# Optimization experiments

Hardware: AMD Instinct MI355X
Metric: run time of the kernel (lower is better)

The kernel has to match this reference:

```python
import jax, jax.numpy as jnp
import numpy as np


def _block(x, src, dst, edge_attr, Wl, bl, Wu, bu):
    # PyG MessagePassing (flow source_to_target): x_i = x[dst], x_j = x[src]
    z = jnp.concatenate([x[dst], x[src], edge_attr], axis=-1)
    m = jax.nn.leaky_relu(z @ Wl + bl)  # default negative_slope = 0.01
    agg = jax.ops.segment_sum(m, dst, num_segments=x.shape[0])  # aggr='add'
    return agg + x @ Wu + bu  # residual upsample


def _rodrigues(axis, ang):
    # axis [...,3] (unit), ang [...] -> rotation matrices [...,3,3]
    ax, ay, az = axis[..., 0], axis[..., 1], axis[..., 2]
    zero = jnp.zeros_like(ax)
    K = jnp.stack([
        jnp.stack([zero, -az, ay], axis=-1),
        jnp.stack([az, zero, -ax], axis=-1),
        jnp.stack([-ay, ax, zero], axis=-1),
    ], axis=-2)
    s = jnp.sin(ang)[..., None, None]
    c = jnp.cos(ang)[..., None, None]
    I = jnp.eye(3, dtype=axis.dtype)
    return I + s * K + (1.0 - c) * (K @ K)


def _fk(ang, parent, offset, G, axis):
    # axis-angle forward kinematics over G graphs of J joints each
    J = ang.shape[0] // G
    a = ang.reshape(G, J)
    ax = axis.reshape(G, J, 3)
    off = offset.reshape(G, J, 3)
    par = parent.reshape(G, J)
    Rl = _rodrigues(ax, a)  # [G,J,3,3] local rotations
    gid = jnp.arange(G)
    pos = jnp.zeros((G, J, 3), ang.dtype)
    rot = jnp.zeros((G, J, 3, 3), ang.dtype)
    for j in range(J):  # J=18 fixed, parents topologically ordered
        p = par[:, j]
        root = (p < 0)[:, None]
        ps = jnp.clip(p, 0, J - 1)
        pr = rot[gid, ps]  # [G,3,3]
        pp = pos[gid, ps]  # [G,3]
        rj = jnp.where(root[..., None], Rl[:, j], pr @ Rl[:, j])
        pj = jnp.where(root, off[:, j], pp + jnp.einsum('gij,gj->gi', pr, off[:, j]))
        rot = rot.at[:, j].set(rj)
        pos = pos.at[:, j].set(pj)
    return pos.reshape(G * J, 3)


def setup_inputs():
    key = jax.random.key(0)
    ks = jax.random.split(key, 48)
    B, Js, Es, Jt, Et = 8192, 17, 16, 18, 17
    f32 = jnp.float32

    def rn(k, shape, scale=1.0):
        return jax.random.normal(k, shape, dtype=f32) * scale

    def lin(k, fin, fout):
        k1, k2 = jax.random.split(k)
        s = 1.0 / float(np.sqrt(fin))
        return rn(k1, (fin, fout), s), rn(k2, (fout,), s)

    offs = np.arange(B)[:, None]
    js = np.arange(Es)
    ei_s = jnp.asarray(np.stack([(offs * Js + js).ravel(), (offs * Js + js + 1).ravel()]), dtype=jnp.int32)
    jt = np.arange(Et)
    ei_t = jnp.asarray(np.stack([(offs * Jt + jt).ravel(), (offs * Jt + jt + 1).ravel()]), dtype=jnp.int32)
    parent = jnp.asarray(np.tile(np.arange(-1, Jt - 1), B), dtype=jnp.int32)
    u = jax.random.uniform(ks[0], (B * Jt, 1), dtype=f32) * 1.5 + 0.1
    axis = rn(ks[1], (B * Jt, 3))
    axis = axis / (jnp.linalg.norm(axis, axis=-1, keepdims=True) + 1e-8)

    inp = {
        'l_hand_x': rn(ks[2], (B * Js, 3)),
        'r_hand_x': rn(ks[3], (B * Js, 3)),
        'l_hand_edge_index': ei_s,
        'r_hand_edge_index': ei_s,
        'l_hand_edge_attr': rn(ks[4], (B * Es, 3)),
        'r_hand_edge_attr': rn(ks[5], (B * Es, 3)),
        'hand_edge_index': ei_t,
        'hand_edge_attr': rn(ks[6], (B * Et, 6)),
        'hand_lower': -u,
        'hand_upper': u,
        'hand_offset': rn(ks[7], (B * Jt, 3), 0.05),
        'hand_parent': parent,
        'hand_axis': axis,
        'num_graphs': B,
    }
    blocks = [('enc1', 3, 16, 3), ('enc2', 16, 32, 3), ('enc3', 32, 64, 3),
              ('dec1', 66, 32, 6), ('dec2', 32, 16, 6), ('dec3', 16, 1, 6)]
    i = 8
    for nm, cin, cout, ed in blocks:
        w, b = lin(ks[i], 2 * cin + ed, cout); i += 1
        inp[nm + '_lw'], inp[nm + '_lb'] = w, b
        w, b = lin(ks[i], cin, cout); i += 1
        inp[nm + '_uw'], inp[nm + '_ub'] = w, b
    w, b = lin(ks[i], Js * 64, Jt * 64)
    inp['trans_w'], inp['trans_b'] = w, b
    return inp


def reference(l_hand_x, r_hand_x, l_hand_edge_index, r_hand_edge_index, l_hand_edge_attr, r_hand_edge_attr, hand_edge_index, hand_edge_attr, hand_lower, hand_upper, hand_offset, hand_parent, hand_axis, num_graphs, enc1_lw, enc1_lb, enc1_uw, enc1_ub, enc2_lw, enc2_lb, enc2_uw, enc2_ub, enc3_lw, enc3_lb, enc3_uw, enc3_ub, trans_w, trans_b, dec1_lw, dec1_lb, dec1_uw, dec1_ub, dec2_lw, dec2_lb, dec2_uw, dec2_ub, dec3_lw, dec3_lb, dec3_uw, dec3_ub):
    # ---- encode ----
    x = jnp.concatenate([l_hand_x, r_hand_x], axis=0)
    ei = jnp.concatenate([l_hand_edge_index, r_hand_edge_index + l_hand_x.shape[0]], axis=1)
    ea = jnp.concatenate([l_hand_edge_attr, r_hand_edge_attr], axis=0)
    s, d = ei[0], ei[1]
    h = _block(x, s, d, ea, enc1_lw, enc1_lb, enc1_uw, enc1_ub)
    h = _block(h, s, d, ea, enc2_lw, enc2_lb, enc2_uw, enc2_ub)
    h = _block(h, s, d, ea, enc3_lw, enc3_lb, enc3_uw, enc3_ub)
    G2 = 2 * num_graphs
    z = jnp.tanh(h.reshape(G2, -1) @ trans_w + trans_b).reshape(-1, 64)
    # ---- decode ----
    half = z.shape[0] // 2
    ei2 = jnp.concatenate([hand_edge_index, hand_edge_index + half], axis=1)
    ea2 = jnp.concatenate([hand_edge_attr, hand_edge_attr], axis=0)
    lo = jnp.concatenate([hand_lower, hand_lower], axis=0)
    up = jnp.concatenate([hand_upper, hand_upper], axis=0)
    off = jnp.concatenate([hand_offset, hand_offset], axis=0)
    par = jnp.concatenate([hand_parent, hand_parent], axis=0)
    ax = jnp.concatenate([hand_axis, hand_axis], axis=0)
    s2, d2 = ei2[0], ei2[1]
    xd = jnp.concatenate([z, lo, up], axis=1)  # [2B*18, 66]
    hd = _block(xd, s2, d2, ea2, dec1_lw, dec1_lb, dec1_uw, dec1_ub)
    hd = _block(hd, s2, d2, ea2, dec2_lw, dec2_lb, dec2_uw, dec2_ub)
    hd = jnp.tanh(_block(hd, s2, d2, ea2, dec3_lw, dec3_lb, dec3_uw, dec3_ub))
    ang = lo + (up - lo) * (hd + 1.0) / 2.0
    pos = _fk(ang, par, off, G2, ax)
    hn = ang.shape[0] // 2
    return (z, ang[:hn], pos[:hn], ang[hn:], pos[hn:])
```

## Files before the change

### kernel.cpp

```cpp
#include <hip/hip_runtime.h>
#include <hip/hip_bf16.h>
#include <stdint.h>


#define ZSIZE 18874368
#define AHALF 147456
#define PHALF 442368

#define WS_AE 0
#define WS_WT 35651584
#define WS_PACK 38158336

#define P_E1 0
#define P_E2 1280
#define P_E3 5888
#define P_D1 19200
#define P_D2 29952

using f32x4 = __attribute__((ext_vector_type(4))) float;
using f16x8 = __attribute__((ext_vector_type(8))) _Float16;
using f16x4 = __attribute__((ext_vector_type(4))) _Float16;

__device__ __forceinline__ float tanh_fast(float x) {
    x = fminf(40.f, fmaxf(-40.f, x));
    float e = __expf(2.f * x);
    return (e - 1.f) * __builtin_amdgcn_rcpf(e + 1.f);
}
__device__ __forceinline__ float lrelu(float x) { return x > 0.f ? x : 0.01f * x; }

__device__ __forceinline__ void gload_lds16(const void* g, void* l) {
    __builtin_amdgcn_global_load_lds(
        (__attribute__((address_space(1))) unsigned int*)g,
        (__attribute__((address_space(3))) unsigned int*)l, 16, 0, 0);
}

__global__ __launch_bounds__(256) void prep_all(
    _Float16* __restrict__ P,
    const float* __restrict__ W, _Float16* __restrict__ Wt,
    const float* __restrict__ e1l, const float* __restrict__ e1u,
    const float* __restrict__ e2l, const float* __restrict__ e2u,
    const float* __restrict__ e3l, const float* __restrict__ e3u,
    const float* __restrict__ d1l, const float* __restrict__ d1u,
    const float* __restrict__ d2l, const float* __restrict__ d2u)
{
    __shared__ float t[32][33];
    const int b = blockIdx.x;
    const int tid = threadIdx.x;

    if (b < 260) {
        const int p = b / 52;
        const int e = (b - p * 52) * 256 + tid;
        int Np, Kp, KpP, N, din, ed, K0, off; const float *Wl, *Wu;
        switch (p) {
          case 0:  Np=32;  Kp=32;  KpP=40;  N=16; din=3;  ed=3; K0=8;  off=P_E1; Wl=e1l; Wu=e1u; break;
          case 1:  Np=64;  Kp=64;  KpP=72;  N=32; din=16; ed=3; K0=24; off=P_E2; Wl=e2l; Wu=e2u; break;
          case 2:  Np=128; Kp=96;  KpP=104; N=64; din=32; ed=3; K0=40; off=P_E3; Wl=e3l; Wu=e3u; break;
          case 3:  Np=64;  Kp=160; KpP=168; N=32; din=66; ed=6; K0=72; off=P_D1; Wl=d1l; Wu=d1u; break;
          default: Np=32;  Kp=96;  KpP=104; N=16; din=32; ed=6; K0=40; off=P_D2; Wl=d2l; Wu=d2u; break;
        }
        if (e >= Np * KpP) return;
        const int n = e / KpP, k = e - n * KpP;
        float v = 0.f;
        if (k < Kp) {
            if (n < N) {
                if (k < din)                          v = Wl[k * N + n];
                else if (k >= K0 && k < K0 + din)     v = Wl[(din + k - K0) * N + n];
                else if (k >= 2*K0 && k < 2*K0 + ed)  v = Wl[(2*din + k - 2*K0) * N + n];
            } else {
                if (k < din) v = Wu[k * N + (n - N)];
            }
        }
        P[off + e] = (_Float16)v;
    } else {
        const int pb = b - 260;
        const int bx = pb % 34, by = pb / 34;
        const int k0 = bx * 32, n0 = by * 32;
        const int tx = tid & 31, ty = tid >> 5;
        for (int i = ty; i < 32; i += 8)
            t[i][tx] = W[(size_t)(k0 + i) * 1152 + n0 + tx];
        __syncthreads();
        for (int i = ty; i < 32; i += 8)
            Wt[(size_t)(n0 + i) * 1088 + k0 + tx] = (_Float16)t[tx][i];
    }
}

#define E_SX 0
#define E_EA 1280
#define E_H1 3840
#define E_H2 7680
#define E_WQ 14080

__global__ __launch_bounds__(256) void enc_kernel(
    const float* __restrict__ lx,  const float* __restrict__ rx,
    const float* __restrict__ lea, const float* __restrict__ rea,
    const float* __restrict__ b1l, const float* __restrict__ b1u,
    const float* __restrict__ b2l, const float* __restrict__ b2u,
    const float* __restrict__ b3l, const float* __restrict__ b3u,
    const _Float16* __restrict__ pack,
    _Float16* __restrict__ Ae)
{
    __shared__ __align__(16) _Float16 sm[27392];
    __shared__ float sb[224];

    const int tid = threadIdx.x;
    const int wave = tid >> 6, lane = tid & 63;
    const int quad = lane >> 4, l16 = lane & 15;
    const int g2b = blockIdx.x * 8;

    for (int i = tid; i < 7040; i += 256) ((uint32_t*)sm)[i] = 0u;
    { uint4* d = (uint4*)&sm[E_WQ]; const uint4* s = (const uint4*)(pack + P_E1);
      for (int i = tid; i < 736; i += 256) d[i] = s[i]; }
    for (int i = tid; i < 16; i += 256) { sb[i] = b1l[i]; sb[16 + i] = b1u[i]; }
    for (int i = tid; i < 32; i += 256) { sb[32 + i] = b2l[i]; sb[64 + i] = b2u[i]; }
    for (int i = tid; i < 64; i += 256) { sb[96 + i] = b3l[i]; sb[160 + i] = b3u[i]; }
    __syncthreads();

    const float* xs = (g2b < 8192) ? lx  + (size_t)g2b * 51 : rx  + (size_t)(g2b - 8192) * 51;
    const float* es = (g2b < 8192) ? lea + (size_t)g2b * 48 : rea + (size_t)(g2b - 8192) * 48;
    for (int i = tid; i < 408; i += 256) {
        int g = i / 51, j = i - g * 51, node = j / 3, c = j - node * 3;
        sm[E_SX + (g * 20 + node) * 8 + c] = (_Float16)xs[i];
    }
    for (int i = tid; i < 384; i += 256) {
        int g = i / 48, j = i - g * 48, node = j / 3, c = j - node * 3;
        sm[E_EA + (g * 20 + node) * 16 + c] = (_Float16)es[i];
    }
    __syncthreads();

    int mts[3] = { wave, wave + 4, wave + 8 };
    const bool has[3] = { true, true, wave < 2 };
    int gN[3], ndN[3], npN[3];
    #pragma unroll
    for (int t = 0; t < 3; t++) {
        const int r16 = mts[t] * 16 + l16;
        gN[t] = r16 / 20; ndN[t] = r16 - gN[t] * 20;
        npN[t] = ndN[t] ? ndN[t] - 1 : 0;
    }

    {
        f32x4 acc[3][2];
        #pragma unroll
        for (int t = 0; t < 3; t++)
            #pragma unroll
            for (int n = 0; n < 2; n++)
                #pragma unroll
                for (int r = 0; r < 4; r++) acc[t][n][r] = 0.f;
        f16x8 bfr[2];
        #pragma unroll
        for (int nt = 0; nt < 2; nt++)
            bfr[nt] = *(const f16x8*)&sm[E_WQ + (nt * 16 + l16) * 40 + quad * 8];
        #pragma unroll
        for (int t = 0; t < 3; t++) if (has[t]) {
            const int aD = E_SX + (gN[t] * 20 + ndN[t]) * 8;
            const int aS = E_SX + (gN[t] * 20 + npN[t]) * 8;
            const int aE = E_EA + (gN[t] * 20 + npN[t]) * 16;
            const int ch = quad;
            const int off = ch < 1 ? aD : (ch < 2 ? aS : aE + (ch - 2) * 8);
            f16x8 af = *(const f16x8*)&sm[off];
            #pragma unroll
            for (int nt = 0; nt < 2; nt++)
                acc[t][nt] = __builtin_amdgcn_mfma_f32_16x16x32_f16(af, bfr[nt], acc[t][nt], 0, 0, 0);
        }
        const int f = l16;
        #pragma unroll
        for (int t = 0; t < 3; t++) if (has[t]) {
            #pragma unroll
            for (int r = 0; r < 4; r++) {
                const int row = mts[t] * 16 + quad * 4 + r;
                const int g = row / 20, nd = row - g * 20;
                if (nd < 17) {
                    const float msg = acc[t][0][r] + sb[f];
                    const float u   = acc[t][1][r] + sb[16 + f];
                    sm[E_H1 + (g * 20 + nd) * 24 + f] =
                        (_Float16)(u + (nd ? lrelu(msg) : 0.f));
                }
            }
        }
    }
    __syncthreads();

    {
        f32x4 acc[3][4];
        #pragma unroll
        for (int t = 0; t < 3; t++)
            #pragma unroll
            for (int n = 0; n < 4; n++)
                #pragma unroll
                for (int r = 0; r < 4; r++) acc[t][n][r] = 0.f;
        #pragma unroll
        for (int Kt = 0; Kt < 2; Kt++) {
            f16x8 bfr[4];
            #pragma unroll
            for (int nt = 0; nt < 4; nt++)
                bfr[nt] = *(const f16x8*)&sm[E_WQ + 1280 + (nt * 16 + l16) * 72 + Kt * 32 + quad * 8];
            #pragma unroll
            for (int t = 0; t < 3; t++) if (has[t]) {
                const int aD = E_H1 + (gN[t] * 20 + ndN[t]) * 24;
                const int aS = E_H1 + (gN[t] * 20 + npN[t]) * 24;
                const int aE = E_EA + (gN[t] * 20 + npN[t]) * 16;
                const int ch = Kt * 4 + quad;
                const int off = ch < 3 ? aD + ch * 8
                              : (ch < 6 ? aS + (ch - 3) * 8 : aE + (ch - 6) * 8);
                f16x8 af = *(const f16x8*)&sm[off];
                #pragma unroll
                for (int nt = 0; nt < 4; nt++)
                    acc[t][nt] = __builtin_amdgcn_mfma_f32_16x16x32_f16(af, bfr[nt], acc[t][nt], 0, 0, 0);
            }
        }
        #pragma unroll
        for (int ntm = 0; ntm < 2; ntm++) {
            const int f = ntm * 16 + l16;
            #pragma unroll
            for (int t = 0; t < 3; t++) if (has[t]) {
                #pragma unroll
                for (int r = 0; r < 4; r++) {
                    const int row = mts[t] * 16 + quad * 4 + r;
                    const int g = row / 20, nd = row - g * 20;
                    if (nd < 17) {
                        const float msg = acc[t][ntm][r]     + sb[32 + f];
                        const float u   = acc[t][ntm + 2][r] + sb[64 + f];
                        sm[E_H2 + (g * 20 + nd) * 40 + f] =
                            (_Float16)(u + (nd ? lrelu(msg) : 0.f));
                    }
                }
            }
        }
    }
    __syncthreads();
    { uint4* d = (uint4*)&sm[E_WQ]; const uint4* s = (const uint4*)(pack + P_E3);
      for (int i = tid; i < 1664; i += 256) d[i] = s[i]; }
    __syncthreads();

    {
        f32x4 acc[3][8];
        #pragma unroll
        for (int t = 0; t < 3; t++)
            #pragma unroll
            for (int n = 0; n < 8; n++)
                #pragma unroll
                for (int r = 0; r < 4; r++) acc[t][n][r] = 0.f;
        #pragma unroll
        for (int Kt = 0; Kt < 3; Kt++) {
            f16x8 bfr[8];
            #pragma unroll
            for (int nt = 0; nt < 8; nt++)
                bfr[nt] = *(const f16x8*)&sm[E_WQ + (nt * 16 + l16) * 104 + Kt * 32 + quad * 8];
            #pragma unroll
            for (int t = 0; t < 3; t++) if (has[t]) {
                const int aD = E_H2 + (gN[t] * 20 + ndN[t]) * 40;
                const int aS = E_H2 + (gN[t] * 20 + npN[t]) * 40;
                const int aE = E_EA + (gN[t] * 20 + npN[t]) * 16;
                const int ch = Kt * 4 + quad;
                const int off = ch < 5 ? aD + ch * 8
                              : (ch < 10 ? aS + (ch - 5) * 8 : aE + (ch - 10) * 8);
                f16x8 af = *(const f16x8*)&sm[off];
                #pragma unroll
                for (int nt = 0; nt < 8; nt++)
                    acc[t][nt] = __builtin_amdgcn_mfma_f32_16x16x32_f16(af, bfr[nt], acc[t][nt], 0, 0, 0);
            }
        }
        #pragma unroll
        for (int ntm = 0; ntm < 4; ntm++) {
            const int f = ntm * 16 + l16;
            #pragma unroll
            for (int t = 0; t < 3; t++) if (has[t]) {
                #pragma unroll
                for (int r = 0; r < 4; r++) {
                    const int row = mts[t] * 16 + quad * 4 + r;
                    const int g = row / 20, nd = row - g * 20;
                    if (nd < 17) {
                        const float msg = acc[t][ntm][r]     + sb[96 + f];
                        const float u   = acc[t][ntm + 4][r] + sb[160 + f];
                        Ae[(size_t)(g2b + g) * 1088 + nd * 64 + f] =
                            (_Float16)(u + (nd ? lrelu(msg) : 0.f));
                    }
                }
            }
        }
    }
}

__global__ __launch_bounds__(256) void trans_gemm(
    const _Float16* __restrict__ A, const _Float16* __restrict__ Bt,
    const float* __restrict__ bias, float* __restrict__ Z)
{
    __shared__ __align__(16) _Float16 As[3][128 * 32];
    __shared__ __align__(16) _Float16 Bs[3][128 * 32];
    const int tid = threadIdx.x;

    const int id = blockIdx.x;
    const int swz = (id & 7) * 144 + (id >> 3);
    const int bm = (swz / 9) * 128, bn = (swz % 9) * 128;

    const int lane = tid & 63, wave = tid >> 6;
    const int wr = wave >> 1, wc = wave & 1;
    const int quad = lane >> 4, l16 = lane & 15;

    const int row0 = wave * 32 + (lane >> 2);
    const int row1 = row0 + 16;
    const int q0 = (lane & 3) ^ ((row0 >> 1) & 3);
    const int q1 = (lane & 3) ^ ((row1 >> 1) & 3);
    const size_t gA0 = (size_t)(bm + row0) * 1088 + q0 * 8;
    const size_t gA1 = (size_t)(bm + row1) * 1088 + q1 * 8;
    const size_t gB0 = (size_t)(bn + row0) * 1088 + q0 * 8;
    const size_t gB1 = (size_t)(bn + row1) * 1088 + q1 * 8;
    const int ldsA0 = (wave * 32) * 32;
    const int ldsA1 = (wave * 32 + 16) * 32;

    int offA[4], offB[4];
    #pragma unroll
    for (int i = 0; i < 4; i++) {
        const int ma = wr * 64 + i * 16 + l16;
        offA[i] = ma * 32 + (quad ^ ((ma >> 1) & 3)) * 8;
        const int nb = wc * 64 + i * 16 + l16;
        offB[i] = nb * 32 + (quad ^ ((nb >> 1) & 3)) * 8;
    }

    f32x4 acc[4][4];
    #pragma unroll
    for (int i = 0; i < 4; i++)
        #pragma unroll
        for (int j = 0; j < 4; j++)
            #pragma unroll
            for (int r = 0; r < 4; r++) acc[i][j][r] = 0.f;

    gload_lds16(A + gA0,       &As[0][ldsA0]);
    gload_lds16(A + gA1,       &As[0][ldsA1]);
    gload_lds16(Bt + gB0,      &Bs[0][ldsA0]);
    gload_lds16(Bt + gB1,      &Bs[0][ldsA1]);
    gload_lds16(A + gA0 + 32,  &As[1][ldsA0]);
    gload_lds16(A + gA1 + 32,  &As[1][ldsA1]);
    gload_lds16(Bt + gB0 + 32, &Bs[1][ldsA0]);
    gload_lds16(Bt + gB1 + 32, &Bs[1][ldsA1]);

    int cb = 0;
    int sb = 2;
    for (int t = 0; t < 34; ++t) {
        if (t < 33) asm volatile("s_waitcnt vmcnt(4)" ::: "memory");
        else        asm volatile("s_waitcnt vmcnt(0)" ::: "memory");
        __builtin_amdgcn_s_barrier();
        if (t + 2 < 34) {
            const int k0 = (t + 2) * 32;
            gload_lds16(A + gA0 + k0,  &As[sb][ldsA0]);
            gload_lds16(A + gA1 + k0,  &As[sb][ldsA1]);
            gload_lds16(Bt + gB0 + k0, &Bs[sb][ldsA0]);
            gload_lds16(Bt + gB1 + k0, &Bs[sb][ldsA1]);
        }
        f16x8 af[4], bfr[4];
        #pragma unroll
        for (int mi = 0; mi < 4; mi++) af[mi]  = *(const f16x8*)&As[cb][offA[mi]];
        #pragma unroll
        for (int ni = 0; ni < 4; ni++) bfr[ni] = *(const f16x8*)&Bs[cb][offB[ni]];
        #pragma unroll
        for (int mi = 0; mi < 4; mi++)
            #pragma unroll
            for (int ni = 0; ni < 4; ni++)
                acc[mi][ni] = __builtin_amdgcn_mfma_f32_16x16x32_f16(
                    af[mi], bfr[ni], acc[mi][ni], 0, 0, 0);
        cb = (cb == 2) ? 0 : cb + 1;
        sb = (sb == 2) ? 0 : sb + 1;
    }

    #pragma unroll
    for (int mi = 0; mi < 4; mi++) {
        #pragma unroll
        for (int ni = 0; ni < 4; ni++) {
            const int n = bn + wc * 64 + ni * 16 + l16;
            const float bv = bias[n];
            #pragma unroll
            for (int r = 0; r < 4; r++) {
                const int m = bm + wr * 64 + mi * 16 + quad * 4 + r;
                Z[(size_t)m * 1152 + n] = tanh_fast(acc[mi][ni][r] + bv);
            }
        }
    }
}

#define D_XD 0
#define D_EA 11520
#define D_H1 14080
#define D_H2 20480
#define D_WQ 23040
#define SB_B1L 0
#define SB_B1U 32
#define SB_B2L 64
#define SB_B2U 80
#define SB_W3L 96
#define SB_W3U 134
#define SB_B3L 150
#define SB_B3U 151
#define SB_ANG 152

__global__ __launch_bounds__(256) void dec_kernel(
    const float* __restrict__ Zc,  const float* __restrict__ tea,
    const float* __restrict__ lo_, const float* __restrict__ up_,
    const float* __restrict__ off_, const int* __restrict__ par_,
    const float* __restrict__ ax_,
    const float* __restrict__ b1l, const float* __restrict__ b1u,
    const float* __restrict__ b2l, const float* __restrict__ b2u,
    const float* __restrict__ w3l, const float* __restrict__ b3l,
    const float* __restrict__ w3u, const float* __restrict__ b3u,
    const _Float16* __restrict__ pack,
    float* __restrict__ out)
{
    __shared__ __align__(16) _Float16 sm[37120];
    __shared__ __align__(16) float sfl[296];
    __shared__ __align__(16) float s_ax[432];
    __shared__ __align__(16) float s_off[432];
    __shared__ __align__(16) float s_lo[144];
    __shared__ __align__(16) float s_up[144];

    const int tid = threadIdx.x;
    const int wave = tid >> 6, lane = tid & 63;
    const int quad = lane >> 4, l16 = lane & 15;
    const int g2b = blockIdx.x * 8;
    const int hb = g2b & 8191;

    for (int i = tid; i < 11520; i += 256) ((uint32_t*)sm)[i] = 0u;
    { uint4* d = (uint4*)&sm[D_WQ]; const uint4* s = (const uint4*)(pack + P_D1);
      for (int i = tid; i < 1760; i += 256) d[i] = s[i]; }
    for (int i = tid; i < 32; i += 256) { sfl[SB_B1L + i] = b1l[i]; sfl[SB_B1U + i] = b1u[i]; }
    for (int i = tid; i < 16; i += 256) { sfl[SB_B2L + i] = b2l[i]; sfl[SB_B2U + i] = b2u[i];
                                          sfl[SB_W3U + i] = w3u[i]; }
    for (int i = tid; i < 38; i += 256) sfl[SB_W3L + i] = w3l[i];
    if (tid == 0) { sfl[SB_B3L] = b3l[0]; sfl[SB_B3U] = b3u[0]; }

    {
        const f32x4* axv = (const f32x4*)(ax_  + (size_t)hb * 54);
        const f32x4* ofv = (const f32x4*)(off_ + (size_t)hb * 54);
        for (int i = tid; i < 108; i += 256) {
            ((f32x4*)s_ax)[i]  = axv[i];
            ((f32x4*)s_off)[i] = ofv[i];
        }
        const f32x4* lov = (const f32x4*)(lo_ + (size_t)hb * 18);
        const f32x4* upv = (const f32x4*)(up_ + (size_t)hb * 18);
        for (int i = tid; i < 36; i += 256) {
            ((f32x4*)s_lo)[i] = lov[i];
            ((f32x4*)s_up)[i] = upv[i];
        }
    }
    __syncthreads();

    {
        const f32x4* Zv = (const f32x4*)(Zc + (size_t)g2b * 1152);
        for (int i = tid; i < 2304; i += 256) {
            const f32x4 v = Zv[i];
            const int g = i / 288, rem = i - g * 288;
            const int node = rem >> 4, c = (rem & 15) << 2;
            f16x4 h;
            h[0] = (_Float16)v[0]; h[1] = (_Float16)v[1];
            h[2] = (_Float16)v[2]; h[3] = (_Float16)v[3];
            *(f16x4*)&sm[D_XD + (g * 20 + node) * 72 + c] = h;
        }
        for (int i = tid; i < 144; i += 256) {
            const int g = i / 18, node = i - g * 18;
            sm[D_XD + (g * 20 + node) * 72 + 64] = (_Float16)s_lo[i];
            sm[D_XD + (g * 20 + node) * 72 + 65] = (_Float16)s_up[i];
        }
        const f32x4* Ev = (const f32x4*)(tea + (size_t)hb * 102);
        for (int i = tid; i < 204; i += 256) {
            const f32x4 v = Ev[i];
            #pragma unroll
            for (int e = 0; e < 4; e++) {
                const int f = 4 * i + e;
                const int g = f / 102, j = f - 102 * g;
                const int node = j / 6, c = j - node * 6;
                sm[D_EA + (g * 20 + node) * 16 + c] = (_Float16)v[e];
            }
        }
    }
    __syncthreads();

    int mts[3] = { wave, wave + 4, wave + 8 };
    const bool has[3] = { true, true, wave < 2 };
    int gN[3], ndN[3], npN[3];
    #pragma unroll
    for (int t = 0; t < 3; t++) {
        const int r16 = mts[t] * 16 + l16;
        gN[t] = r16 / 20; ndN[t] = r16 - gN[t] * 20;
        npN[t] = ndN[t] ? ndN[t] - 1 : 0;
    }

    {
        f32x4 acc[3][4];
        #pragma unroll
        for (int t = 0; t < 3; t++)
            #pragma unroll
            for (int n = 0; n < 4; n++)
                #pragma unroll
                for (int r = 0; r < 4; r++) acc[t][n][r] = 0.f;
        #pragma unroll
        for (int Kt = 0; Kt < 5; Kt++) {
            f16x8 bfr[4];
            #pragma unroll
            for (int nt = 0; nt < 4; nt++)
                bfr[nt] = *(const f16x8*)&sm[D_WQ + (nt * 16 + l16) * 168 + Kt * 32 + quad * 8];
            #pragma unroll
            for (int t = 0; t < 3; t++) if (has[t]) {
                const int aD = D_XD + (gN[t] * 20 + ndN[t]) * 72;
                const int aS = D_XD + (gN[t] * 20 + npN[t]) * 72;
                const int aE = D_EA + (gN[t] * 20 + npN[t]) * 16;
                const int ch = Kt * 4 + quad;
                const int off = ch < 9 ? aD + ch * 8
                              : (ch < 18 ? aS + (ch - 9) * 8 : aE + (ch - 18) * 8);
                f16x8 af = *(const f16x8*)&sm[off];
                #pragma unroll
                for (int nt = 0; nt < 4; nt++)
                    acc[t][nt] = __builtin_amdgcn_mfma_f32_16x16x32_f16(af, bfr[nt], acc[t][nt], 0, 0, 0);
            }
        }
        #pragma unroll
        for (int ntm = 0; ntm < 2; ntm++) {
            const int f = ntm * 16 + l16;
            #pragma unroll
            for (int t = 0; t < 3; t++) if (has[t]) {
                #pragma unroll
                for (int r = 0; r < 4; r++) {
                    const int row = mts[t] * 16 + quad * 4 + r;
                    const int g = row / 20, nd = row - g * 20;
                    if (nd < 18) {
                        const float msg = acc[t][ntm][r]     + sfl[SB_B1L + f];
                        const float u   = acc[t][ntm + 2][r] + sfl[SB_B1U + f];
                        sm[D_H1 + (g * 20 + nd) * 40 + f] =
                            (_Float16)(u + (nd ? lrelu(msg) : 0.f));
                    }
                }
            }
        }
    }
    __syncthreads();

    {
        f32x4 acc[3][2];
        #pragma unroll
        for (int t = 0; t < 3; t++)
            #pragma unroll
            for (int n = 0; n < 2; n++)
                #pragma unroll
                for (int r = 0; r < 4; r++) acc[t][n][r] = 0.f;
        #pragma unroll
        for (int Kt = 0; Kt < 3; Kt++) {
            f16x8 bfr[2];
            #pragma unroll
            for (int nt = 0; nt < 2; nt++)
                bfr[nt] = *(const f16x8*)&sm[D_WQ + 10752 + (nt * 16 + l16) * 104 + Kt * 32 + quad * 8];
            #pragma unroll
            for (int t = 0; t < 3; t++) if (has[t]) {
                const int aD = D_H1 + (gN[t] * 20 + ndN[t]) * 40;
                const int aS = D_H1 + (gN[t] * 20 + npN[t]) * 40;
                const int aE = D_EA + (gN[t] * 20 + npN[t]) * 16;
                const int ch = Kt * 4 + quad;
                const int off = ch < 5 ? aD + ch * 8
                              : (ch < 10 ? aS + (ch - 5) * 8 : aE + (ch - 10) * 8);
                f16x8 af = *(const f16x8*)&sm[off];
                #pragma unroll
                for (int nt = 0; nt < 2; nt++)
                    acc[t][nt] = __builtin_amdgcn_mfma_f32_16x16x32_f16(af, bfr[nt], acc[t][nt], 0, 0, 0);
            }
        }
        const int f = l16;
        #pragma unroll
        for (int t = 0; t < 3; t++) if (has[t]) {
            #pragma unroll
            for (int r = 0; r < 4; r++) {
                const int row = mts[t] * 16 + quad * 4 + r;
                const int g = row / 20, nd = row - g * 20;
                if (nd < 18) {
                    const float msg = acc[t][0][r] + sfl[SB_B2L + f];
                    const float u   = acc[t][1][r] + sfl[SB_B2U + f];
                    sm[D_H2 + (g * 20 + nd) * 16 + f] =
                        (_Float16)(u + (nd ? lrelu(msg) : 0.f));
                }
            }
        }
    }
    __syncthreads();

    if (tid < 144) {
        const int g = tid / 18, nd = tid - (tid / 18) * 18;
        const _Float16* hn = &sm[D_H2 + (g * 20 + nd) * 16];
        float acc = sfl[SB_B3U];
        #pragma unroll
        for (int c = 0; c < 16; c++) acc += (float)hn[c] * sfl[SB_W3U + c];
        if (nd > 0) {
            const _Float16* hp = &sm[D_H2 + (g * 20 + nd - 1) * 16];
            const _Float16* e  = &sm[D_EA + (g * 20 + nd - 1) * 16];
            float m = sfl[SB_B3L];
            #pragma unroll
            for (int c = 0; c < 16; c++) m += (float)hn[c] * sfl[SB_W3L + c];
            #pragma unroll
            for (int c = 0; c < 16; c++) m += (float)hp[c] * sfl[SB_W3L + 16 + c];
            #pragma unroll
            for (int c = 0; c < 6;  c++) m += (float)e[c]  * sfl[SB_W3L + 32 + c];
            acc += lrelu(m);
        }
        const float hd = tanh_fast(acc);
        const int g2 = g2b + g;
        const float lo = s_lo[tid], up = s_up[tid];
        const float ang = lo + (up - lo) * (hd + 1.f) * 0.5f;
        sfl[SB_ANG + tid] = ang;
        const size_t abase = (g2 < 8192) ? (size_t)ZSIZE + (size_t)g2 * 18
                                         : (size_t)ZSIZE + AHALF + PHALF + (size_t)(g2 - 8192) * 18;
        out[abase + nd] = ang;
    }
    __syncthreads();

    if (tid < 24) {
        const int g = tid / 3, r = tid - (tid / 3) * 3;
        const int g2 = g2b + g;
        const size_t pbase = (g2 < 8192)
            ? (size_t)ZSIZE + AHALF + (size_t)g2 * 54
            : (size_t)ZSIZE + AHALF + PHALF + AHALF + (size_t)(g2 - 8192) * 54;
        float Rr0 = 0.f, Rr1 = 0.f, Rr2 = 0.f, pr = 0.f;
        #pragma unroll
        for (int j = 0; j < 18; j++) {
            const int m = g * 18 + j;
            const float a0 = s_ax[m * 3 + 0], a1 = s_ax[m * 3 + 1], a2 = s_ax[m * 3 + 2];
            const float o0 = s_off[m * 3 + 0], o1 = s_off[m * 3 + 1], o2 = s_off[m * 3 + 2];
            float s, c;
            __sincosf(sfl[SB_ANG + m], &s, &c);
            const float omc = 1.f - c;
            const float n2 = a0 * a0 + a1 * a1 + a2 * a2;
            const float dg = 1.f - omc * n2;
            const float L00 = dg + omc * a0 * a0;
            const float L01 = omc * a0 * a1 - s * a2;
            const float L02 = omc * a0 * a2 + s * a1;
            const float L10 = omc * a1 * a0 + s * a2;
            const float L11 = dg + omc * a1 * a1;
            const float L12 = omc * a1 * a2 - s * a0;
            const float L20 = omc * a2 * a0 - s * a1;
            const float L21 = omc * a2 * a1 + s * a0;
            const float L22 = dg + omc * a2 * a2;
            if (j == 0) {
                Rr0 = (r == 0) ? L00 : ((r == 1) ? L10 : L20);
                Rr1 = (r == 0) ? L01 : ((r == 1) ? L11 : L21);
                Rr2 = (r == 0) ? L02 : ((r == 1) ? L12 : L22);
                pr  = (r == 0) ? o0  : ((r == 1) ? o1  : o2);
            } else {
                pr += Rr0 * o0 + Rr1 * o1 + Rr2 * o2;
                const float t0 = Rr0 * L00 + Rr1 * L10 + Rr2 * L20;
                const float t1 = Rr0 * L01 + Rr1 * L11 + Rr2 * L21;
                const float t2 = Rr0 * L02 + Rr1 * L12 + Rr2 * L22;
                Rr0 = t0; Rr1 = t1; Rr2 = t2;
            }
            out[pbase + j * 3 + r] = pr;
        }
    }
}

extern "C" void kernel_launch(void* const* d_in, const int* in_sizes, int n_in,
                              void* d_out, int out_size, void* d_ws, size_t ws_size,
                              hipStream_t stream)
{
    int i_tw, i_tb, i_d1, i_d2, i_d3;
    if (n_in > 27 && in_sizes[26] == 1088 * 1152) {
        i_tw = 26; i_tb = 27; i_d1 = 28; i_d2 = 32; i_d3 = 36;
    } else {
        i_d1 = 26; i_d2 = 30; i_d3 = 34; i_tw = 38; i_tb = 39;
    }
    auto fp = [&](int i) { return (const float*)d_in[i]; };

    _Float16* Ae   = (_Float16*)((char*)d_ws + WS_AE);
    _Float16* Wt   = (_Float16*)((char*)d_ws + WS_WT);
    _Float16* Pack = (_Float16*)((char*)d_ws + WS_PACK);

    prep_all<<<1484, 256, 0, stream>>>(
        Pack, fp(i_tw), Wt,
        fp(14), fp(16), fp(18), fp(20), fp(22), fp(24),
        fp(i_d1), fp(i_d1 + 2), fp(i_d2), fp(i_d2 + 2));

    enc_kernel<<<2048, 256, 0, stream>>>(
        fp(0), fp(1), fp(4), fp(5),
        fp(15), fp(17), fp(19), fp(21), fp(23), fp(25),
        Pack, Ae);

    trans_gemm<<<1152, 256, 0, stream>>>(Ae, Wt, fp(i_tb), (float*)d_out);

    dec_kernel<<<2048, 256, 0, stream>>>(
        (const float*)d_out, fp(7), fp(8), fp(9), fp(10),
        (const int*)d_in[11], fp(12),
        fp(i_d1 + 1), fp(i_d1 + 3), fp(i_d2 + 1), fp(i_d2 + 3),
        fp(i_d3), fp(i_d3 + 1), fp(i_d3 + 2), fp(i_d3 + 3),
        Pack, (float*)d_out);
}
```

Baseline: 345.1 us.

## Load trans_gemm B operand directly into registers with double buffering instead of LDS

In the trans_gemm kernel, the B (weight) tile no longer goes through shared memory. Each wave reads its B fragments straight from global memory into registers, using two alternating register sets. The K loop is unrolled by two so the next B fragments load while the current MFMAs run. This cuts LDS footprint and LDS read/write traffic for B, but waves sharing a column tile now fetch duplicate B data from global/L2, and the vmcnt waits become harder to reason about.

```diff
diff --git a/kernel.cpp b/kernel.cpp
--- a/kernel.cpp
+++ b/kernel.cpp
@@ -285,7 +285,6 @@
     const float* __restrict__ bias, float* __restrict__ Z)
 {
     __shared__ __align__(16) _Float16 As[3][128 * 32];
-    __shared__ __align__(16) _Float16 Bs[3][128 * 32];
     const int tid = threadIdx.x;
 
     const int id = blockIdx.x;
@@ -302,18 +301,17 @@
     const int q1 = (lane & 3) ^ ((row1 >> 1) & 3);
     const size_t gA0 = (size_t)(bm + row0) * 1088 + q0 * 8;
     const size_t gA1 = (size_t)(bm + row1) * 1088 + q1 * 8;
-    const size_t gB0 = (size_t)(bn + row0) * 1088 + q0 * 8;
-    const size_t gB1 = (size_t)(bn + row1) * 1088 + q1 * 8;
     const int ldsA0 = (wave * 32) * 32;
     const int ldsA1 = (wave * 32 + 16) * 32;
 
-    int offA[4], offB[4];
+    int offA[4];
+    size_t gB[4];
     #pragma unroll
     for (int i = 0; i < 4; i++) {
         const int ma = wr * 64 + i * 16 + l16;
         offA[i] = ma * 32 + (quad ^ ((ma >> 1) & 3)) * 8;
         const int nb = wc * 64 + i * 16 + l16;
-        offB[i] = nb * 32 + (quad ^ ((nb >> 1) & 3)) * 8;
+        gB[i] = (size_t)(bn + nb) * 1088 + quad * 8;
     }
 
     f32x4 acc[4][4];
@@ -324,39 +322,73 @@
             #pragma unroll
             for (int r = 0; r < 4; r++) acc[i][j][r] = 0.f;
 
-    gload_lds16(A + gA0,       &As[0][ldsA0]);
-    gload_lds16(A + gA1,       &As[0][ldsA1]);
-    gload_lds16(Bt + gB0,      &Bs[0][ldsA0]);
-    gload_lds16(Bt + gB1,      &Bs[0][ldsA1]);
-    gload_lds16(A + gA0 + 32,  &As[1][ldsA0]);
-    gload_lds16(A + gA1 + 32,  &As[1][ldsA1]);
-    gload_lds16(Bt + gB0 + 32, &Bs[1][ldsA0]);
-    gload_lds16(Bt + gB1 + 32, &Bs[1][ldsA1]);
+    gload_lds16(A + gA0,      &As[0][ldsA0]);
+    gload_lds16(A + gA1,      &As[0][ldsA1]);
+    gload_lds16(A + gA0 + 32, &As[1][ldsA0]);
+    gload_lds16(A + gA1 + 32, &As[1][ldsA1]);
+    __builtin_amdgcn_sched_barrier(0);
+    f16x8 b0[4], b1[4];
+    #pragma unroll
+    for (int ni = 0; ni < 4; ni++) b0[ni] = *(const f16x8*)&Bt[gB[ni]];
+    __builtin_amdgcn_sched_barrier(0);
 
     int cb = 0;
     int sb = 2;
-    for (int t = 0; t < 34; ++t) {
-        if (t < 33) asm volatile("s_waitcnt vmcnt(4)" ::: "memory");
-        else        asm volatile("s_waitcnt vmcnt(0)" ::: "memory");
+    for (int it = 0; it < 17; ++it) {
+        const int s0 = 2 * it, s1 = s0 + 1;
+        asm volatile("s_waitcnt vmcnt(6)" ::: "memory");
         __builtin_amdgcn_s_barrier();
-        if (t + 2 < 34) {
-            const int k0 = (t + 2) * 32;
-            gload_lds16(A + gA0 + k0,  &As[sb][ldsA0]);
-            gload_lds16(A + gA1 + k0,  &As[sb][ldsA1]);
-            gload_lds16(Bt + gB0 + k0, &Bs[sb][ldsA0]);
-            gload_lds16(Bt + gB1 + k0, &Bs[sb][ldsA1]);
-        }
-        f16x8 af[4], bfr[4];
-        #pragma unroll
-        for (int mi = 0; mi < 4; mi++) af[mi]  = *(const f16x8*)&As[cb][offA[mi]];
-        #pragma unroll
-        for (int ni = 0; ni < 4; ni++) bfr[ni] = *(const f16x8*)&Bs[cb][offB[ni]];
-        #pragma unroll
-        for (int mi = 0; mi < 4; mi++)
-            #pragma unroll
-            for (int ni = 0; ni < 4; ni++)
-                acc[mi][ni] = __builtin_amdgcn_mfma_f32_16x16x32_f16(
-                    af[mi], bfr[ni], acc[mi][ni], 0, 0, 0);
+        if (s0 + 2 < 34) {
+            const int kn = (s0 + 2) * 32;
+            gload_lds16(A + gA0 + kn, &As[sb][ldsA0]);
+            gload_lds16(A + gA1 + kn, &As[sb][ldsA1]);
+        }
+        __builtin_amdgcn_sched_barrier(0);
+        {
+            const int kb = s1 * 32;
+            #pragma unroll
+            for (int ni = 0; ni < 4; ni++) b1[ni] = *(const f16x8*)&Bt[gB[ni] + kb];
+        }
+        __builtin_amdgcn_sched_barrier(0);
+        {
+            f16x8 af[4];
+            #pragma unroll
+            for (int mi = 0; mi < 4; mi++) af[mi] = *(const f16x8*)&As[cb][offA[mi]];
+            #pragma unroll
+            for (int mi = 0; mi < 4; mi++)
+                #pragma unroll
+                for (int ni = 0; ni < 4; ni++)
+                    acc[mi][ni] = __builtin_amdgcn_mfma_f32_16x16x32_f16(
+                        af[mi], b0[ni], acc[mi][ni], 0, 0, 0);
+        }
+        cb = (cb == 2) ? 0 : cb + 1;
+        sb = (sb == 2) ? 0 : sb + 1;
+
+        asm volatile("s_waitcnt vmcnt(6)" ::: "memory");
+        __builtin_amdgcn_s_barrier();
+        if (s1 + 2 < 34) {
+            const int kn = (s1 + 2) * 32;
+            gload_lds16(A + gA0 + kn, &As[sb][ldsA0]);
+            gload_lds16(A + gA1 + kn, &As[sb][ldsA1]);
+        }
+        __builtin_amdgcn_sched_barrier(0);
+        if (s1 + 1 < 34) {
+            const int kb = (s1 + 1) * 32;
+            #pragma unroll
+            for (int ni = 0; ni < 4; ni++) b0[ni] = *(const f16x8*)&Bt[gB[ni] + kb];
+        }
+        __builtin_amdgcn_sched_barrier(0);
+        {
+            f16x8 af[4];
+            #pragma unroll
+            for (int mi = 0; mi < 4; mi++) af[mi] = *(const f16x8*)&As[cb][offA[mi]];
+            #pragma unroll
+            for (int mi = 0; mi < 4; mi++)
+                #pragma unroll
+                for (int ni = 0; ni < 4; ni++)
+                    acc[mi][ni] = __builtin_amdgcn_mfma_f32_16x16x32_f16(
+                        af[mi], b1[ni], acc[mi][ni], 0, 0, 0);
+        }
         cb = (cb == 2) ? 0 : cb + 1;
         sb = (sb == 2) ? 0 : sb + 1;
     }
```

After: 384.8 us. +11.5%, slower.
